# Optimization experiments

Hardware: AMD Instinct MI355X
Metric: run time of the kernel (lower is better)

## Reference

```python
import jax, jax.numpy as jnp
import numpy as np

N_SRC = 100000
N_DST = 100000
E = 1250000
IN_SRC = 64
IN_DST = 64
OUT = 64


def setup_inputs() -> dict:
    key = jax.random.key(0)
    k = jax.random.split(key, 7)
    x_src = jax.random.normal(k[0], (N_SRC, IN_SRC), dtype=jnp.float32)
    x_dst = jax.random.normal(k[1], (N_DST, IN_DST), dtype=jnp.float32)
    edge_index_sd = jax.random.randint(k[2], (2, E), 0, N_SRC, dtype=jnp.int64)
    edge_weight = jax.random.uniform(k[3], (E,), dtype=jnp.float32)
    # Linear params (torch: y = x @ W.T + b), kaiming-ish scale
    W_nei = jax.random.normal(k[4], (OUT, IN_SRC), dtype=jnp.float32) / np.sqrt(IN_SRC)
    W_self = jax.random.normal(k[5], (OUT, IN_DST), dtype=jnp.float32) / np.sqrt(IN_DST)
    b_self = jax.random.normal(k[6], (OUT,), dtype=jnp.float32) / np.sqrt(IN_DST)
    return {"x_src": x_src, "x_dst": x_dst, "edge_index_sd": edge_index_sd,
            "edge_weight": edge_weight, "W_nei": W_nei, "W_self": W_self,
            "b_self": b_self}


def reference(x_src, x_dst, edge_index_sd, edge_weight, W_nei, W_self, b_self):
    src_idx = edge_index_sd[0]
    dst_idx = edge_index_sd[1]
    # self term: [N_dst, out]
    out = x_dst @ W_self.T + b_self
    # neighbor transform then gather per edge: [E, out]
    h_src = x_src @ W_nei.T
    msg = h_src[src_idx] * edge_weight[:, None]
    # scatter-add into dst rows
    out = out.at[dst_idx].add(msg)
    return out
```

## Files before the change

kernel.cpp:

```cpp
#include <hip/hip_runtime.h>

#define NN 100000
#define FD 64
#define NE 1250000

#define RPB 64
#define NBK ((NN + RPB - 1) / RPB)
#define NBP 2048
#define CAP 1024
#define CH  8192
#define NCH ((NE + CH - 1) / CH)
#define NTILE (NN / 16)

#define TPW 2
#define NWM (NTILE / TPW)
#define LIN_GRID ((2 * NWM + 3) / 4)
#define NEI_GRID ((NWM + 3) / 4)

#define SLP 68

typedef __attribute__((ext_vector_type(8))) short bf16x8;
typedef __attribute__((ext_vector_type(4))) float f32x4;

__device__ __forceinline__ short cvt_bf16(float f) {
    unsigned u = __float_as_uint(f);
    return (short)((u + 0x7FFFu + ((u >> 16) & 1u)) >> 16);
}
__device__ __forceinline__ float bf2f(unsigned short u) {
    return __uint_as_float(((unsigned)u) << 16);
}
__device__ __forceinline__ bf16x8 cvt8(const float4& a, const float4& b) {
    bf16x8 f;
    f[0]=cvt_bf16(a.x); f[1]=cvt_bf16(a.y); f[2]=cvt_bf16(a.z); f[3]=cvt_bf16(a.w);
    f[4]=cvt_bf16(b.x); f[5]=cvt_bf16(b.y); f[6]=cvt_bf16(b.z); f[7]=cvt_bf16(b.w);
    return f;
}

__global__ __launch_bounds__(256) void lin_nei(
    const float* __restrict__ x_src, const float* __restrict__ W_nei,
    unsigned short* __restrict__ hbuf, int* __restrict__ gcur)
{
    if (blockIdx.x == 0) {
        #pragma unroll
        for (int i = 0; i < NBP / 256; i++) gcur[threadIdx.x + i * 256] = 0;
    }
    const int lane = threadIdx.x & 63;
    const int m    = lane & 15;
    const int quad = lane >> 4;
    const int gw   = blockIdx.x * 4 + (threadIdx.x >> 6);
    if (gw >= NWM) return;

    const float* xb = x_src + (size_t)(gw * (TPW * 16) + m) * FD;
    float4 xv[TPW][4];
    #pragma unroll
    for (int t = 0; t < TPW; t++) {
        const float* xr = xb + (size_t)t * 16 * FD;
        xv[t][0] = *(const float4*)(xr + quad * 8);
        xv[t][1] = *(const float4*)(xr + quad * 8 + 4);
        xv[t][2] = *(const float4*)(xr + 32 + quad * 8);
        xv[t][3] = *(const float4*)(xr + 32 + quad * 8 + 4);
    }
    bf16x8 wf[2][4];
    #pragma unroll
    for (int kc = 0; kc < 2; kc++) {
        #pragma unroll
        for (int ct = 0; ct < 4; ct++) {
            const float4 w0 = *(const float4*)(W_nei + (ct * 16 + m) * FD + kc * 32 + quad * 8);
            const float4 w1 = *(const float4*)(W_nei + (ct * 16 + m) * FD + kc * 32 + quad * 8 + 4);
            wf[kc][ct] = cvt8(w0, w1);
        }
    }
    #pragma unroll
    for (int t = 0; t < TPW; t++) {
        const bf16x8 a0 = cvt8(xv[t][0], xv[t][1]);
        const bf16x8 a1 = cvt8(xv[t][2], xv[t][3]);
        const size_t rowbase = (size_t)(gw * (TPW * 16) + t * 16 + m) * FD;
        #pragma unroll
        for (int ct = 0; ct < 4; ct++) {
            f32x4 z = (f32x4){0.f, 0.f, 0.f, 0.f};
            z = __builtin_amdgcn_mfma_f32_16x16x32_bf16(wf[0][ct], a0, z, 0, 0, 0);
            z = __builtin_amdgcn_mfma_f32_16x16x32_bf16(wf[1][ct], a1, z, 0, 0, 0);
            ushort4 sv;
            sv.x = (unsigned short)cvt_bf16(z[0]);
            sv.y = (unsigned short)cvt_bf16(z[1]);
            sv.z = (unsigned short)cvt_bf16(z[2]);
            sv.w = (unsigned short)cvt_bf16(z[3]);
            *(ushort4*)(hbuf + rowbase + ct * 16 + quad * 4) = sv;
        }
    }
}

__global__ __launch_bounds__(1024) void kplace(
    const int* __restrict__ src, const int* __restrict__ dst,
    const float* __restrict__ ew, int* __restrict__ gcursor,
    int2* __restrict__ sp)
{
    __shared__ int cnt[NBP];
    const int t = threadIdx.x;
    #pragma unroll
    for (int i = 0; i < NBP / 1024; i++) cnt[t + i * 1024] = 0;
    __syncthreads();
    const int e0 = blockIdx.x * CH;

    int d[8];
    #pragma unroll
    for (int k = 0; k < 8; k++) {
        const int e = e0 + t + k * 1024;
        d[k] = (e < NE) ? dst[e] : -1;
    }
    #pragma unroll
    for (int k = 0; k < 8; k++)
        if (d[k] >= 0) atomicAdd(&cnt[d[k] >> 6], 1);
    __syncthreads();

    #pragma unroll
    for (int i = 0; i < NBP / 1024; i++) {
        const int bb = t + i * 1024;
        const int c = cnt[bb];
        cnt[bb] = c ? (bb * CAP + atomicAdd(&gcursor[bb], c)) : 0;
    }
    __syncthreads();

    int s[8]; float w[8];
    #pragma unroll
    for (int k = 0; k < 8; k++) {
        const int e = e0 + t + k * 1024;
        if (e < NE) { s[k] = src[e]; w[k] = ew[e]; }
    }
    #pragma unroll
    for (int k = 0; k < 8; k++) {
        if (d[k] >= 0) {
            const int p = atomicAdd(&cnt[d[k] >> 6], 1);
            sp[p] = make_int2(s[k] | ((d[k] & (RPB - 1)) << 17),
                              __float_as_int(w[k]));
        }
    }
}

__global__ __launch_bounds__(256) void sort_gather(
    const int2* __restrict__ sp, const int* __restrict__ gcursor,
    const unsigned short* __restrict__ h, const float* __restrict__ x_dst,
    const float* __restrict__ W_self, const float* __restrict__ b_self,
    float* __restrict__ out)
{
    __shared__ int2 ebuf[CAP + 16];
    __shared__ int hist[RPB];
    __shared__ int rs[RPB];
    __shared__ int cur[RPB];
    __shared__ float self_lds[RPB * SLP];
    const int t = threadIdx.x;
    const int b = blockIdx.x;
    const int cnt = gcursor[b];
    const int s0 = b * CAP;
    const int row0 = b * RPB;
    const int wv   = t >> 6;
    const int lane = t & 63;
    const int m    = lane & 15;
    const int quad = lane >> 4;

    int xrow = row0 + wv * 16 + m;
    if (xrow >= NN) xrow = NN - 1;
    const float* xr = x_dst + (size_t)xrow * FD;
    const float4 x0 = *(const float4*)(xr + quad * 8);
    const float4 x1 = *(const float4*)(xr + quad * 8 + 4);
    const float4 x2 = *(const float4*)(xr + 32 + quad * 8);
    const float4 x3 = *(const float4*)(xr + 32 + quad * 8 + 4);

    if (t < RPB) hist[t] = 0;

    int2 ev[4]; int er[4];
    #pragma unroll
    for (int k = 0; k < 4; k++) {
        const int j = t + k * 256;
        if (j < cnt) { ev[k] = sp[s0 + j]; er[k] = ev[k].x >> 17; }
        else er[k] = -1;
    }
    __syncthreads();
    #pragma unroll
    for (int k = 0; k < 4; k++)
        if (er[k] >= 0) atomicAdd(&hist[er[k]], 1);
    __syncthreads();
    if (t < 64) {
        const int v = hist[t];
        int inc = v;
        #pragma unroll
        for (int off = 1; off < 64; off <<= 1) {
            int u = __shfl_up(inc, off, 64);
            if (t >= off) inc += u;
        }
        rs[t]  = inc - v;
        cur[t] = inc - v;
    }
    __syncthreads();
    #pragma unroll
    for (int k = 0; k < 4; k++) {
        if (er[k] >= 0) {
            const int p = atomicAdd(&cur[er[k]], 1);
            ebuf[p] = ev[k];
        }
    }
    if (t < 16) ebuf[cnt + t] = make_int2(0, 0);

    {
        const bf16x8 a0 = cvt8(x0, x1);
        const bf16x8 a1 = cvt8(x2, x3);
        #pragma unroll
        for (int ct = 0; ct < 4; ct++) {
            const float* wr = W_self + (ct * 16 + m) * FD;
            const float4 w0 = *(const float4*)(wr + quad * 8);
            const float4 w1 = *(const float4*)(wr + quad * 8 + 4);
            const float4 w2 = *(const float4*)(wr + 32 + quad * 8);
            const float4 w3 = *(const float4*)(wr + 32 + quad * 8 + 4);
            f32x4 z = (f32x4){0.f, 0.f, 0.f, 0.f};
            z = __builtin_amdgcn_mfma_f32_16x16x32_bf16(cvt8(w0, w1), a0, z, 0, 0, 0);
            z = __builtin_amdgcn_mfma_f32_16x16x32_bf16(cvt8(w2, w3), a1, z, 0, 0, 0);
            const float4 bb = *(const float4*)(b_self + ct * 16 + quad * 4);
            float4 v;
            v.x = z[0] + bb.x; v.y = z[1] + bb.y;
            v.z = z[2] + bb.z; v.w = z[3] + bb.w;
            *(float4*)&self_lds[(wv * 16 + m) * SLP + ct * 16 + quad * 4] = v;
        }
    }
    __syncthreads();

    const unsigned tb = (unsigned)m << 3;
    #pragma unroll
    for (int i = 0; i < 4; i++) {
        const int r   = i * 16 + wv * 4 + quad;
        const int row = row0 + r;
        const int rsr = rs[r];
        const int n   = hist[r];
        float a0 = 0.f, a1 = 0.f, a2 = 0.f, a3 = 0.f;
        for (int k = 0; k < n; k += 8) {
            int2 ed[8];
            #pragma unroll
            for (int j = 0; j < 8; j++)
                ed[j] = ebuf[rsr + k + j];
            uint2 dv[8]; float w8[8];
            #pragma unroll
            for (int j = 0; j < 8; j++) {
                const unsigned off = (((unsigned)(ed[j].x & 0x1FFFF)) << 7) | tb;
                dv[j] = *(const uint2*)((const char*)h + off);
                w8[j] = (k + j < n) ? __int_as_float(ed[j].y) : 0.f;
            }
            #pragma unroll
            for (int j = 0; j < 8; j++) {
                const float w = w8[j];
                a0 = fmaf(__uint_as_float(dv[j].x << 16),         w, a0);
                a1 = fmaf(__uint_as_float(dv[j].x & 0xFFFF0000u), w, a1);
                a2 = fmaf(__uint_as_float(dv[j].y << 16),         w, a2);
                a3 = fmaf(__uint_as_float(dv[j].y & 0xFFFF0000u), w, a3);
            }
        }
        if (row < NN) {
            const float4 sv = *(const float4*)&self_lds[r * SLP + (m << 2)];
            float4 v;
            v.x = sv.x + a0; v.y = sv.y + a1; v.z = sv.z + a2; v.w = sv.w + a3;
            *(float4*)(out + (size_t)row * FD + (m << 2)) = v;
        }
    }
}

__global__ __launch_bounds__(256) void lin_both(
    const float* __restrict__ x_src, const float* __restrict__ x_dst,
    const float* __restrict__ W_nei, const float* __restrict__ W_self,
    const float* __restrict__ b_self, unsigned short* __restrict__ hbuf,
    float* __restrict__ out)
{
    const int lane = threadIdx.x & 63;
    const int m    = lane & 15;
    const int quad = lane >> 4;
    const int gw   = blockIdx.x * 4 + (threadIdx.x >> 6);
    if (gw >= 2 * NWM) return;
    const bool self = gw >= NWM;
    const int  wm   = self ? gw - NWM : gw;
    const float* __restrict__ x = self ? x_dst : x_src;
    const float* __restrict__ W = self ? W_self : W_nei;

    const float* xb = x + (size_t)(wm * (TPW * 16) + m) * FD;
    float4 xv[TPW][4];
    #pragma unroll
    for (int t = 0; t < TPW; t++) {
        const float* xr = xb + (size_t)t * 16 * FD;
        xv[t][0] = *(const float4*)(xr + quad * 8);
        xv[t][1] = *(const float4*)(xr + quad * 8 + 4);
        xv[t][2] = *(const float4*)(xr + 32 + quad * 8);
        xv[t][3] = *(const float4*)(xr + 32 + quad * 8 + 4);
    }
    bf16x8 wf[2][4];
    #pragma unroll
    for (int kc = 0; kc < 2; kc++) {
        #pragma unroll
        for (int ct = 0; ct < 4; ct++) {
            const float4 w0 = *(const float4*)(W + (ct * 16 + m) * FD + kc * 32 + quad * 8);
            const float4 w1 = *(const float4*)(W + (ct * 16 + m) * FD + kc * 32 + quad * 8 + 4);
            wf[kc][ct] = cvt8(w0, w1);
        }
    }
    float4 bv[4];
    if (self) {
        #pragma unroll
        for (int ct = 0; ct < 4; ct++)
            bv[ct] = *(const float4*)(b_self + ct * 16 + quad * 4);
    }
    #pragma unroll
    for (int t = 0; t < TPW; t++) {
        const bf16x8 a0 = cvt8(xv[t][0], xv[t][1]);
        const bf16x8 a1 = cvt8(xv[t][2], xv[t][3]);
        f32x4 acc[4];
        #pragma unroll
        for (int ct = 0; ct < 4; ct++) {
            f32x4 zz = (f32x4){0.f, 0.f, 0.f, 0.f};
            zz = __builtin_amdgcn_mfma_f32_16x16x32_bf16(wf[0][ct], a0, zz, 0, 0, 0);
            zz = __builtin_amdgcn_mfma_f32_16x16x32_bf16(wf[1][ct], a1, zz, 0, 0, 0);
            acc[ct] = zz;
        }
        const size_t rowbase = (size_t)(wm * (TPW * 16) + t * 16 + m) * FD;
        if (!self) {
            #pragma unroll
            for (int ct = 0; ct < 4; ct++) {
                ushort4 sv;
                sv.x = (unsigned short)cvt_bf16(acc[ct][0]);
                sv.y = (unsigned short)cvt_bf16(acc[ct][1]);
                sv.z = (unsigned short)cvt_bf16(acc[ct][2]);
                sv.w = (unsigned short)cvt_bf16(acc[ct][3]);
                *(ushort4*)(hbuf + rowbase + ct * 16 + quad * 4) = sv;
            }
        } else {
            #pragma unroll
            for (int ct = 0; ct < 4; ct++) {
                float4 v;
                v.x = acc[ct][0] + bv[ct].x;
                v.y = acc[ct][1] + bv[ct].y;
                v.z = acc[ct][2] + bv[ct].z;
                v.w = acc[ct][3] + bv[ct].w;
                *(float4*)(out + rowbase + ct * 16 + quad * 4) = v;
            }
        }
    }
}

__global__ __launch_bounds__(256) void scatter_edges(
    const unsigned short* __restrict__ h, const int* __restrict__ eidx,
    const float* __restrict__ ew, float* __restrict__ out)
{
    const int lane  = threadIdx.x & 63;
    const int gwave = (int)((blockIdx.x * blockDim.x + threadIdx.x) >> 6);
    const int nwave = (int)((gridDim.x * blockDim.x) >> 6);
    const int* __restrict__ src = eidx;
    const int* __restrict__ dst = eidx + NE;
    for (int e = gwave; e < NE; e += nwave) {
        const float v = bf2f(h[(size_t)src[e] * FD + lane]) * ew[e];
        atomicAdd(out + (size_t)dst[e] * FD + lane, v);
    }
}

extern "C" void kernel_launch(void* const* d_in, const int* in_sizes, int n_in,
                              void* d_out, int out_size, void* d_ws, size_t ws_size,
                              hipStream_t stream)
{
    const float* x_src  = (const float*)d_in[0];
    const float* x_dst  = (const float*)d_in[1];
    const int*   eidx   = (const int*)  d_in[2];
    const float* ew     = (const float*)d_in[3];
    const float* W_nei  = (const float*)d_in[4];
    const float* W_self = (const float*)d_in[5];
    const float* b_self = (const float*)d_in[6];
    float* out = (float*)d_out;

    const int* src = eidx;
    const int* dst = eidx + NE;

    char* ws = (char*)d_ws;
    size_t off = 0;
    auto alloc = [&](size_t bytes) { char* p = ws + off; off += (bytes + 15) & ~(size_t)15; return p; };
    unsigned short* h = (unsigned short*)alloc((size_t)NN * FD * sizeof(unsigned short));
    int*  gcursor  = (int*) alloc((size_t)NBP * sizeof(int));
    int2* sp       = (int2*)alloc((size_t)NBP * CAP * sizeof(int2));
    const size_t need_main = off;
    const size_t need_h    = (size_t)NN * FD * sizeof(unsigned short);

    if (ws_size >= need_main) {
        lin_nei<<<NEI_GRID, 256, 0, stream>>>(x_src, W_nei, h, gcursor);
        kplace<<<NCH, 1024, 0, stream>>>(src, dst, ew, gcursor, sp);
        sort_gather<<<NBK, 256, 0, stream>>>(sp, gcursor, h, x_dst,
                                             W_self, b_self, out);
    } else if (ws_size >= need_h) {
        lin_both<<<LIN_GRID, 256, 0, stream>>>(x_src, x_dst, W_nei, W_self,
                                               b_self, h, out);
        scatter_edges<<<2048, 256, 0, stream>>>(h, eidx, ew, out);
    }
}
```

Baseline: 172.8 us.

## Make sort_gather persistent with atomic block stealing and double-buffered gathers

sort_gather becomes a persistent kernel over a fixed grid, where each workgroup repeatedly claims the next 64-row bucket through an atomic counter stored in the last gcursor slot. The per-row gather loop is also double-buffered: it loads the next 8 edges' h rows while doing FMAs on the current 8, so more memory requests are in flight. This relies on gcursor[NBP-1] being zeroed beforehand and unused as a bucket count (NBK is below NBP). The cost is extra registers and an extra barrier per bucket.

Measured after the change: 197.9 us. 14.5% more time.

```diff
diff --git a/kernel.cpp b/kernel.cpp
--- a/kernel.cpp
+++ b/kernel.cpp
@@ -18,6 +18,7 @@
 #define NEI_GRID ((NWM + 3) / 4)
 
 #define SLP 68
+#define SG_GRID 1536
 
 typedef __attribute__((ext_vector_type(8))) short bf16x8;
 typedef __attribute__((ext_vector_type(4))) float f32x4;
@@ -137,8 +138,30 @@
     }
 }
 
+#define LOAD8(dv, wv, basek)                                              \
+    {                                                                      \
+        _Pragma("unroll")                                                  \
+        for (int j = 0; j < 8; j++) {                                      \
+            const int2 ed = ebuf[rsr + (basek) + j];                       \
+            const unsigned off = (((unsigned)(ed.x & 0x1FFFF)) << 7) | tb; \
+            dv[j] = *(const uint2*)((const char*)h + off);                 \
+            wv[j] = ((basek) + j < n) ? __int_as_float(ed.y) : 0.f;        \
+        }                                                                  \
+    }
+#define FMA8(dv, wv)                                                      \
+    {                                                                      \
+        _Pragma("unroll")                                                  \
+        for (int j = 0; j < 8; j++) {                                      \
+            const float w = wv[j];                                         \
+            a0 = fmaf(__uint_as_float(dv[j].x << 16),         w, a0);      \
+            a1 = fmaf(__uint_as_float(dv[j].x & 0xFFFF0000u), w, a1);      \
+            a2 = fmaf(__uint_as_float(dv[j].y << 16),         w, a2);      \
+            a3 = fmaf(__uint_as_float(dv[j].y & 0xFFFF0000u), w, a3);      \
+        }                                                                  \
+    }
+
 __global__ __launch_bounds__(256) void sort_gather(
-    const int2* __restrict__ sp, const int* __restrict__ gcursor,
+    const int2* __restrict__ sp, int* __restrict__ gcursor,
     const unsigned short* __restrict__ h, const float* __restrict__ x_dst,
     const float* __restrict__ W_self, const float* __restrict__ b_self,
     float* __restrict__ out)
@@ -148,116 +171,118 @@
     __shared__ int rs[RPB];
     __shared__ int cur[RPB];
     __shared__ float self_lds[RPB * SLP];
+    __shared__ int curb;
+    int* __restrict__ gsteal = gcursor + (NBP - 1);
     const int t = threadIdx.x;
-    const int b = blockIdx.x;
-    const int cnt = gcursor[b];
-    const int s0 = b * CAP;
-    const int row0 = b * RPB;
     const int wv   = t >> 6;
     const int lane = t & 63;
     const int m    = lane & 15;
     const int quad = lane >> 4;
 
-    int xrow = row0 + wv * 16 + m;
-    if (xrow >= NN) xrow = NN - 1;
-    const float* xr = x_dst + (size_t)xrow * FD;
-    const float4 x0 = *(const float4*)(xr + quad * 8);
-    const float4 x1 = *(const float4*)(xr + quad * 8 + 4);
-    const float4 x2 = *(const float4*)(xr + 32 + quad * 8);
-    const float4 x3 = *(const float4*)(xr + 32 + quad * 8 + 4);
-
-    if (t < RPB) hist[t] = 0;
-
-    int2 ev[4]; int er[4];
-    #pragma unroll
-    for (int k = 0; k < 4; k++) {
-        const int j = t + k * 256;
-        if (j < cnt) { ev[k] = sp[s0 + j]; er[k] = ev[k].x >> 17; }
-        else er[k] = -1;
-    }
-    __syncthreads();
-    #pragma unroll
-    for (int k = 0; k < 4; k++)
-        if (er[k] >= 0) atomicAdd(&hist[er[k]], 1);
-    __syncthreads();
-    if (t < 64) {
-        const int v = hist[t];
-        int inc = v;
-        #pragma unroll
-        for (int off = 1; off < 64; off <<= 1) {
-            int u = __shfl_up(inc, off, 64);
-            if (t >= off) inc += u;
-        }
-        rs[t]  = inc - v;
-        cur[t] = inc - v;
-    }
-    __syncthreads();
-    #pragma unroll
-    for (int k = 0; k < 4; k++) {
-        if (er[k] >= 0) {
-            const int p = atomicAdd(&cur[er[k]], 1);
-            ebuf[p] = ev[k];
-        }
-    }
-    if (t < 16) ebuf[cnt + t] = make_int2(0, 0);
-
-    {
-        const bf16x8 a0 = cvt8(x0, x1);
-        const bf16x8 a1 = cvt8(x2, x3);
-        #pragma unroll
-        for (int ct = 0; ct < 4; ct++) {
-            const float* wr = W_self + (ct * 16 + m) * FD;
-            const float4 w0 = *(const float4*)(wr + quad * 8);
-            const float4 w1 = *(const float4*)(wr + quad * 8 + 4);
-            const float4 w2 = *(const float4*)(wr + 32 + quad * 8);
-            const float4 w3 = *(const float4*)(wr + 32 + quad * 8 + 4);
-            f32x4 z = (f32x4){0.f, 0.f, 0.f, 0.f};
-            z = __builtin_amdgcn_mfma_f32_16x16x32_bf16(cvt8(w0, w1), a0, z, 0, 0, 0);
-            z = __builtin_amdgcn_mfma_f32_16x16x32_bf16(cvt8(w2, w3), a1, z, 0, 0, 0);
-            const float4 bb = *(const float4*)(b_self + ct * 16 + quad * 4);
-            float4 v;
-            v.x = z[0] + bb.x; v.y = z[1] + bb.y;
-            v.z = z[2] + bb.z; v.w = z[3] + bb.w;
-            *(float4*)&self_lds[(wv * 16 + m) * SLP + ct * 16 + quad * 4] = v;
-        }
-    }
-    __syncthreads();
-
-    const unsigned tb = (unsigned)m << 3;
-    #pragma unroll
-    for (int i = 0; i < 4; i++) {
-        const int r   = i * 16 + wv * 4 + quad;
-        const int row = row0 + r;
-        const int rsr = rs[r];
-        const int n   = hist[r];
-        float a0 = 0.f, a1 = 0.f, a2 = 0.f, a3 = 0.f;
-        for (int k = 0; k < n; k += 8) {
-            int2 ed[8];
+    for (;;) {
+        if (t == 0) curb = atomicAdd(gsteal, 1);
+        __syncthreads();
+        const int b = curb;
+        if (b >= NBK) return;
+        const int cnt = gcursor[b];
+        const int s0 = b * CAP;
+        const int row0 = b * RPB;
+
+        int xrow = row0 + wv * 16 + m;
+        if (xrow >= NN) xrow = NN - 1;
+        const float* xr = x_dst + (size_t)xrow * FD;
+        const float4 x0 = *(const float4*)(xr + quad * 8);
+        const float4 x1 = *(const float4*)(xr + quad * 8 + 4);
+        const float4 x2 = *(const float4*)(xr + 32 + quad * 8);
+        const float4 x3 = *(const float4*)(xr + 32 + quad * 8 + 4);
+
+        if (t < RPB) hist[t] = 0;
+
+        int2 ev[4]; int er[4];
+        #pragma unroll
+        for (int k = 0; k < 4; k++) {
+            const int j = t + k * 256;
+            if (j < cnt) { ev[k] = sp[s0 + j]; er[k] = ev[k].x >> 17; }
+            else er[k] = -1;
+        }
+        __syncthreads();
+        #pragma unroll
+        for (int k = 0; k < 4; k++)
+            if (er[k] >= 0) atomicAdd(&hist[er[k]], 1);
+        __syncthreads();
+        if (t < 64) {
+            const int v = hist[t];
+            int inc = v;
             #pragma unroll
-            for (int j = 0; j < 8; j++)
-                ed[j] = ebuf[rsr + k + j];
-            uint2 dv[8]; float w8[8];
+            for (int off = 1; off < 64; off <<= 1) {
+                int u = __shfl_up(inc, off, 64);
+                if (t >= off) inc += u;
+            }
+            rs[t]  = inc - v;
+            cur[t] = inc - v;
+        }
+        __syncthreads();
+        #pragma unroll
+        for (int k = 0; k < 4; k++) {
+            if (er[k] >= 0) {
+                const int p = atomicAdd(&cur[er[k]], 1);
+                ebuf[p] = ev[k];
+            }
+        }
+        if (t < 16) ebuf[cnt + t] = make_int2(0, 0);
+
+        {
+            const bf16x8 a0 = cvt8(x0, x1);
+            const bf16x8 a1 = cvt8(x2, x3);
             #pragma unroll
-            for (int j = 0; j < 8; j++) {
-                const unsigned off = (((unsigned)(ed[j].x & 0x1FFFF)) << 7) | tb;
-                dv[j] = *(const uint2*)((const char*)h + off);
-                w8[j] = (k + j < n) ? __int_as_float(ed[j].y) : 0.f;
-            }
-            #pragma unroll
-            for (int j = 0; j < 8; j++) {
-                const float w = w8[j];
-                a0 = fmaf(__uint_as_float(dv[j].x << 16),         w, a0);
-                a1 = fmaf(__uint_as_float(dv[j].x & 0xFFFF0000u), w, a1);
-                a2 = fmaf(__uint_as_float(dv[j].y << 16),         w, a2);
-                a3 = fmaf(__uint_as_float(dv[j].y & 0xFFFF0000u), w, a3);
-            }
-        }
-        if (row < NN) {
-            const float4 sv = *(const float4*)&self_lds[r * SLP + (m << 2)];
-            float4 v;
-            v.x = sv.x + a0; v.y = sv.y + a1; v.z = sv.z + a2; v.w = sv.w + a3;
-            *(float4*)(out + (size_t)row * FD + (m << 2)) = v;
-        }
+            for (int ct = 0; ct < 4; ct++) {
+                const float* wr = W_self + (ct * 16 + m) * FD;
+                const float4 w0 = *(const float4*)(wr + quad * 8);
+                const float4 w1 = *(const float4*)(wr + quad * 8 + 4);
+                const float4 w2 = *(const float4*)(wr + 32 + quad * 8);
+                const float4 w3 = *(const float4*)(wr + 32 + quad * 8 + 4);
+                f32x4 z = (f32x4){0.f, 0.f, 0.f, 0.f};
+                z = __builtin_amdgcn_mfma_f32_16x16x32_bf16(cvt8(w0, w1), a0, z, 0, 0, 0);
+                z = __builtin_amdgcn_mfma_f32_16x16x32_bf16(cvt8(w2, w3), a1, z, 0, 0, 0);
+                const float4 bb = *(const float4*)(b_self + ct * 16 + quad * 4);
+                float4 v;
+                v.x = z[0] + bb.x; v.y = z[1] + bb.y;
+                v.z = z[2] + bb.z; v.w = z[3] + bb.w;
+                *(float4*)&self_lds[(wv * 16 + m) * SLP + ct * 16 + quad * 4] = v;
+            }
+        }
+        __syncthreads();
+
+        const unsigned tb = (unsigned)m << 3;
+        #pragma unroll
+        for (int i = 0; i < 4; i++) {
+            const int r   = i * 16 + wv * 4 + quad;
+            const int row = row0 + r;
+            const int rsr = rs[r];
+            const int n   = hist[r];
+            float a0 = 0.f, a1 = 0.f, a2 = 0.f, a3 = 0.f;
+            const int nr = (n + 15) >> 4;
+            if (nr > 0) {
+                uint2 dvA[8], dvB[8]; float wA[8], wB[8];
+                LOAD8(dvA, wA, 0);
+                int kk = 0;
+                for (int p = 0; p < nr; p++) {
+                    LOAD8(dvB, wB, kk + 8);
+                    FMA8(dvA, wA);
+                    if (p + 1 < nr) LOAD8(dvA, wA, kk + 16);
+                    FMA8(dvB, wB);
+                    kk += 16;
+                }
+            }
+            if (row < NN) {
+                const float4 sv = *(const float4*)&self_lds[r * SLP + (m << 2)];
+                float4 v;
+                v.x = sv.x + a0; v.y = sv.y + a1;
+                v.z = sv.z + a2; v.w = sv.w + a3;
+                *(float4*)(out + (size_t)row * FD + (m << 2)) = v;
+            }
+        }
+        __syncthreads();
     }
 }
 
@@ -383,8 +408,8 @@
     if (ws_size >= need_main) {
         lin_nei<<<NEI_GRID, 256, 0, stream>>>(x_src, W_nei, h, gcursor);
         kplace<<<NCH, 1024, 0, stream>>>(src, dst, ew, gcursor, sp);
-        sort_gather<<<NBK, 256, 0, stream>>>(sp, gcursor, h, x_dst,
-                                             W_self, b_self, out);
+        sort_gather<<<SG_GRID, 256, 0, stream>>>(sp, gcursor, h, x_dst,
+                                                 W_self, b_self, out);
     } else if (ws_size >= need_h) {
         lin_both<<<LIN_GRID, 256, 0, stream>>>(x_src, x_dst, W_nei, W_self,
                                                b_self, h, out);
```
